# Performance work log

Measured on AMD Instinct MI355X. Metric: run time of the kernel, lower is better.

## Reference

```python
import jax, jax.numpy as jnp
import numpy as np


def setup_inputs() -> dict:
    key = jax.random.key(0)
    M, D = 131072, 16
    x = jax.random.normal(key, (M, D), dtype=jnp.float32)
    return {"x": x, "n_segs": 64, "k": 16}


def reference(x, n_segs, k):
    """Segmented kNN graph: for each point set (segment), find each point's k
    nearest neighbors (L2) within its own segment and emit edges knn -> node,
    with node ids globally offset by the segment start (sum_{p<i} |V_p| + j).

    Returns
    -------
    dists : [M, k] float32  squared L2 distance to each of the k neighbors
    src   : [M, k] int32    global node ids of the k predecessors of each node
    dst   : [M]    int32    global node ids (dst of the k edges in each row)
    """
    M, D = x.shape
    S = M // n_segs  # points per segment (equal-sized segments)
    xs = x.reshape(n_segs, S, D)                              # [N, S, D]
    sq = jnp.sum(xs * xs, axis=-1)                            # [N, S]
    # squared pairwise distances per segment: ||a||^2 + ||b||^2 - 2 a.b
    dist = sq[:, :, None] + sq[:, None, :] - 2.0 * jnp.einsum(
        "nsd,ntd->nst", xs, xs
    )                                                         # [N, S, S]
    neg, idx = jax.lax.top_k(-dist, k)                        # [N, S, k] each
    offs = (jnp.arange(n_segs, dtype=jnp.int32) * S)[:, None, None]
    src = (idx.astype(jnp.int32) + offs).reshape(M, k)        # global neighbor ids
    dst = jnp.arange(M, dtype=jnp.int32)
    dists = (-neg).reshape(M, k)
    return dists, src, dst
```

## Files before the change

kernel.cpp:

```cpp
#include <hip/hip_runtime.h>
#include <math.h>


#define DD 16
#define KK 16
#define SENT 0x7F7FFFFFu

typedef unsigned int uint;
typedef unsigned short ushort;
typedef short bf16x8 __attribute__((ext_vector_type(8)));
typedef float f32x4 __attribute__((ext_vector_type(4)));

__device__ __forceinline__ ushort f2bf(float f) {
  uint u = __float_as_uint(f);
  return (ushort)((u + 0x7FFFu + ((u >> 16) & 1u)) >> 16);
}

__device__ __forceinline__ void bitonic16(uint (&b)[16]) {
#pragma unroll
  for (int s = 8; s >= 1; s >>= 1) {
#pragma unroll
    for (int j = 0; j < 16; ++j) {
      if ((j & s) == 0) {
        uint lo = min(b[j], b[j + s]), hi = max(b[j], b[j + s]);
        b[j] = lo; b[j + s] = hi;
      }
    }
  }
}

__device__ __forceinline__ void flushSlots(uint (&bd)[8], uint (&qd)[4]) {
  qd[1] |= 1u; qd[2] |= 2u; qd[3] |= 3u;
#define CS(i, j) { uint lo = min(qd[i], qd[j]), hi = max(qd[i], qd[j]); qd[i] = lo; qd[j] = hi; }
  CS(0, 1) CS(2, 3) CS(0, 2) CS(1, 3) CS(1, 2)
#undef CS
#pragma unroll
  for (int t = 0; t < 4; ++t) bd[4 + t] = min(bd[4 + t], qd[3 - t]);
#pragma unroll
  for (int s = 4; s >= 1; s >>= 1) {
#pragma unroll
    for (int j = 0; j < 8; ++j) {
      if ((j & s) == 0) {
        uint lo = min(bd[j], bd[j + s]), hi = max(bd[j], bd[j + s]);
        bd[j] = lo; bd[j + s] = hi;
      }
    }
  }
#pragma unroll
  for (int t = 0; t < 4; ++t) qd[t] = SENT;
}

__global__ void sknn_prep(const float* __restrict__ x, ushort* __restrict__ augA,
                          ushort* __restrict__ augB, int M) {
  int p = blockIdx.x * 256 + threadIdx.x;
  if (p >= M) return;
  const float4* r = (const float4*)(x + (size_t)p * DD);
  float4 v0 = r[0], v1 = r[1], v2 = r[2], v3 = r[3];
  float f[16] = {v0.x, v0.y, v0.z, v0.w, v1.x, v1.y, v1.z, v1.w,
                 v2.x, v2.y, v2.z, v2.w, v3.x, v3.y, v3.z, v3.w};
  float sq = 0.f;
#pragma unroll
  for (int d = 0; d < 16; ++d) sq = fmaf(f[d], f[d], sq);
  ushort sq_hi = f2bf(sq);
  float hif = __uint_as_float(((uint)sq_hi) << 16);
  ushort sq_lo = f2bf(sq - hif);

  ushort A[32], B[32];
#pragma unroll
  for (int d = 0; d < 16; ++d) { A[d] = f2bf(-2.f * f[d]); B[d] = f2bf(f[d]); }
  A[16] = 0x3F80; A[17] = 0x3F80; A[18] = sq_hi; A[19] = sq_lo; A[20] = 0x3F80;
  B[16] = sq_hi;  B[17] = sq_lo;  B[18] = 0x3F80; B[19] = 0x3F80; B[20] = 0x3F80;
#pragma unroll
  for (int d = 21; d < 32; ++d) { A[d] = 0; B[d] = 0; }

  uint wa[16], wb[16];
#pragma unroll
  for (int i = 0; i < 16; ++i) {
    wa[i] = (uint)A[2 * i] | ((uint)A[2 * i + 1] << 16);
    wb[i] = (uint)B[2 * i] | ((uint)B[2 * i + 1] << 16);
  }
  uint4* da = (uint4*)(augA + (size_t)p * 32);
  uint4* db = (uint4*)(augB + (size_t)p * 32);
#pragma unroll
  for (int i = 0; i < 4; ++i) {
    da[i] = make_uint4(wa[4 * i], wa[4 * i + 1], wa[4 * i + 2], wa[4 * i + 3]);
    db[i] = make_uint4(wb[4 * i], wb[4 * i + 1], wb[4 * i + 2], wb[4 * i + 3]);
  }
}

__global__ __launch_bounds__(256, 4)
void sknn_mfma(const ushort* __restrict__ augA, const ushort* __restrict__ augB,
               float* __restrict__ out, int M, int S) {
  const int tid  = threadIdx.x;
  const int wv   = tid >> 6;
  const int lane = tid & 63;
  const int r16  = lane & 15;
  const int kh   = lane >> 4;
  const int qbase = blockIdx.x * 64 + wv * 16;
  const int segBase = (blockIdx.x * 64 / S) * S;
  const int NT = S / 16;
  const int NC = NT / 8;

  __shared__ uint shm[4096];

  const bf16x8 bfrag = *(const bf16x8*)(augB + (size_t)(qbase + r16) * 32 + kh * 8);
  const ushort* __restrict__ abase = augA + (size_t)segBase * 32;

  const int src_u = ((lane >> 2) * 32) + ((((lane & 3) ^ ((lane >> 3) & 3))) * 8);
  const int st0 = 2 * wv, st1 = 2 * wv + 1;
  const int rd_u = r16 * 16 + ((kh ^ ((r16 >> 1) & 3)) * 4);

  uint bd[8], qd[4];
#pragma unroll
  for (int i = 0; i < 8; ++i) bd[i] = SENT;
#pragma unroll
  for (int i = 0; i < 4; ++i) qd[i] = SENT;

  const f32x4 zacc = {0.f, 0.f, 0.f, 0.f};
  const uint kmask = 0xFFFFF800u;
  uint vidx = (uint)(kh * 4);

  auto cap = [&](const f32x4& acc) {
#pragma unroll
    for (int e = 0; e < 4; ++e)
      qd[e] = min(qd[e], (__float_as_uint(acc[e]) & kmask) | vidx);
    vidx += 16u;
  };

  {
    uint4 s0 = *(const uint4*)(abase + (size_t)st0 * 512 + src_u);
    uint4 s1 = *(const uint4*)(abase + (size_t)st1 * 512 + src_u);
    *(uint4*)(&shm[st0 * 256 + lane * 4]) = s0;
    *(uint4*)(&shm[st1 * 256 + lane * 4]) = s1;
    __syncthreads();
  }

  for (int c = 0; c < NC; ++c) {
    const uint cur = (uint)(c & 1) * 2048u;
    const uint nxt = 2048u - cur;
    uint4 s0, s1;
    const bool hasNext = (c + 1 < NC);
    if (hasNext) {
      const ushort* cb = abase + (size_t)(c + 1) * 4096;
      s0 = *(const uint4*)(cb + (size_t)st0 * 512 + src_u);
      s1 = *(const uint4*)(cb + (size_t)st1 * 512 + src_u);
    }
    const uint* tb = &shm[cur];
    bf16x8 fA = *(const bf16x8*)(tb + 0 * 256 + rd_u);
    bf16x8 fB = *(const bf16x8*)(tb + 1 * 256 + rd_u);
    bf16x8 fC = *(const bf16x8*)(tb + 2 * 256 + rd_u);
    bf16x8 fD = *(const bf16x8*)(tb + 3 * 256 + rd_u);
    f32x4 c0 = __builtin_amdgcn_mfma_f32_16x16x32_bf16(fA, bfrag, zacc, 0, 0, 0);
    f32x4 c1 = __builtin_amdgcn_mfma_f32_16x16x32_bf16(fB, bfrag, zacc, 0, 0, 0);
    fA = *(const bf16x8*)(tb + 4 * 256 + rd_u);
    fB = *(const bf16x8*)(tb + 5 * 256 + rd_u);
    cap(c0); cap(c1);
    f32x4 c2 = __builtin_amdgcn_mfma_f32_16x16x32_bf16(fC, bfrag, zacc, 0, 0, 0);
    f32x4 c3 = __builtin_amdgcn_mfma_f32_16x16x32_bf16(fD, bfrag, zacc, 0, 0, 0);
    fC = *(const bf16x8*)(tb + 6 * 256 + rd_u);
    fD = *(const bf16x8*)(tb + 7 * 256 + rd_u);
    cap(c2); cap(c3);
    c0 = __builtin_amdgcn_mfma_f32_16x16x32_bf16(fA, bfrag, zacc, 0, 0, 0);
    c1 = __builtin_amdgcn_mfma_f32_16x16x32_bf16(fB, bfrag, zacc, 0, 0, 0);
    cap(c0); cap(c1);
    c2 = __builtin_amdgcn_mfma_f32_16x16x32_bf16(fC, bfrag, zacc, 0, 0, 0);
    c3 = __builtin_amdgcn_mfma_f32_16x16x32_bf16(fD, bfrag, zacc, 0, 0, 0);
    cap(c2); cap(c3);
    flushSlots(bd, qd);
    if (hasNext) {
      *(uint4*)(&shm[nxt + st0 * 256 + lane * 4]) = s0;
      *(uint4*)(&shm[nxt + st1 * 256 + lane * 4]) = s1;
    }
    __syncthreads();
  }

  uint* myrow = &shm[tid * 9];
#pragma unroll
  for (int i = 0; i < 8; ++i) myrow[i] = bd[i];
  __syncthreads();
  if (kh != 0) return;

  uint cur16[16];
  {
    const uint* prow = &shm[(tid + 16) * 9];
#pragma unroll
    for (int i = 0; i < 8; ++i) cur16[i] = bd[i];
#pragma unroll
    for (int i = 0; i < 8; ++i) cur16[8 + i] = prow[7 - i];
    bitonic16(cur16);
  }
#pragma unroll
  for (int c = 2; c < 4; ++c) {
    const uint* prow = &shm[(tid + 16 * c) * 9];
    uint ob[8];
#pragma unroll
    for (int i = 0; i < 8; ++i) ob[i] = prow[i];
#pragma unroll
    for (int q = 0; q < 8; ++q) cur16[8 + q] = min(cur16[8 + q], ob[7 - q]);
    bitonic16(cur16);
  }

  const int p = qbase + r16;
  const float fb = (float)segBase;
  float dv[16], sv[16];
#pragma unroll
  for (int i = 0; i < 16; ++i) {
    dv[i] = __uint_as_float(cur16[i] & 0xFFFFF800u) - 1.0f;
    sv[i] = fb + (float)(cur16[i] & 0x7FFu);
  }
  float* __restrict__ dptr = out + (size_t)p * KK;
  ((float4*)dptr)[0] = make_float4(dv[0], dv[1], dv[2], dv[3]);
  ((float4*)dptr)[1] = make_float4(dv[4], dv[5], dv[6], dv[7]);
  ((float4*)dptr)[2] = make_float4(dv[8], dv[9], dv[10], dv[11]);
  ((float4*)dptr)[3] = make_float4(dv[12], dv[13], dv[14], dv[15]);
  float* __restrict__ sptr = out + (size_t)M * KK + (size_t)p * KK;
  ((float4*)sptr)[0] = make_float4(sv[0], sv[1], sv[2], sv[3]);
  ((float4*)sptr)[1] = make_float4(sv[4], sv[5], sv[6], sv[7]);
  ((float4*)sptr)[2] = make_float4(sv[8], sv[9], sv[10], sv[11]);
  ((float4*)sptr)[3] = make_float4(sv[12], sv[13], sv[14], sv[15]);
  out[(size_t)2 * M * KK + p] = (float)p;
}

__device__ __forceinline__ void flushQ16(uint (&bd)[16], uint (&qd)[4], uint& tau) {
#define CS(i, j) { uint lo = min(qd[i], qd[j]), hi = max(qd[i], qd[j]); qd[i] = lo; qd[j] = hi; }
  CS(0, 1) CS(2, 3) CS(0, 2) CS(1, 3) CS(1, 2)
#undef CS
#pragma unroll
  for (int t = 0; t < 4; ++t) {
    uint m = min(bd[12 + t], qd[3 - t]);
    uint lo = min(bd[4 + t], m), hi = max(bd[4 + t], m);
    bd[4 + t] = lo; bd[12 + t] = hi;
  }
#pragma unroll
  for (int s = 4; s >= 1; s >>= 1) {
#pragma unroll
    for (int j = 0; j < 16; ++j) {
      if ((j & s) == 0) {
        uint lo = min(bd[j], bd[j + s]), hi = max(bd[j], bd[j + s]);
        bd[j] = lo; bd[j + s] = hi;
      }
    }
  }
#pragma unroll
  for (int t = 0; t < 4; ++t) qd[t] = SENT;
  tau = min(tau, bd[15]);
}

__device__ __forceinline__ void merge16(uint (&bd)[16], const uint (&ob)[16]) {
  uint t[16];
#pragma unroll
  for (int i = 0; i < 16; ++i) t[i] = min(bd[i], ob[15 - i]);
#pragma unroll
  for (int i = 0; i < 16; ++i) bd[i] = t[i];
  bitonic16(bd);
}

template <int CLEN_C>
__global__ __launch_bounds__(256, 4)
void sknn_valu(const float* __restrict__ x, uint* __restrict__ part,
               int M, int S, int nch, int clenRt) {
  const int CLEN  = (CLEN_C > 0) ? CLEN_C : clenRt;
  const int tid   = threadIdx.x;
  const int qblk  = blockIdx.x / nch;
  const int chunk = blockIdx.x - qblk * nch;
  const int p     = qblk * 256 + tid;
  const int segBase = ((qblk * 256) / S) * S;
  const int j0    = chunk * CLEN;

  const float4* __restrict__ qr = (const float4*)(x + (size_t)p * DD);
  const float4 q0 = qr[0], q1 = qr[1], q2 = qr[2], q3 = qr[3];

  uint bd[16], qd[4];
  uint tau = SENT;
#pragma unroll
  for (int t = 0; t < 16; ++t) bd[t] = SENT;
#pragma unroll
  for (int t = 0; t < 4; ++t) qd[t] = SENT;

  const float4* __restrict__ cb = (const float4*)(x + (size_t)(segBase + j0) * DD);

  auto proc = [&](float4 c0, float4 c1, float4 c2, float4 c3, int j) {
    float t0, d0, d1, d2, d3;
    t0 = q0.x - c0.x; d0 = t0 * t0;
    t0 = q0.y - c0.y; d0 = fmaf(t0, t0, d0);
    t0 = q0.z - c0.z; d0 = fmaf(t0, t0, d0);
    t0 = q0.w - c0.w; d0 = fmaf(t0, t0, d0);
    t0 = q1.x - c1.x; d1 = t0 * t0;
    t0 = q1.y - c1.y; d1 = fmaf(t0, t0, d1);
    t0 = q1.z - c1.z; d1 = fmaf(t0, t0, d1);
    t0 = q1.w - c1.w; d1 = fmaf(t0, t0, d1);
    t0 = q2.x - c2.x; d2 = t0 * t0;
    t0 = q2.y - c2.y; d2 = fmaf(t0, t0, d2);
    t0 = q2.z - c2.z; d2 = fmaf(t0, t0, d2);
    t0 = q2.w - c2.w; d2 = fmaf(t0, t0, d2);
    t0 = q3.x - c3.x; d3 = t0 * t0;
    t0 = q3.y - c3.y; d3 = fmaf(t0, t0, d3);
    t0 = q3.z - c3.z; d3 = fmaf(t0, t0, d3);
    t0 = q3.w - c3.w; d3 = fmaf(t0, t0, d3);
    float nd = (d0 + d1) + (d2 + d3);
    const uint key = (__float_as_uint(nd) & 0xFFFFF800u) | (uint)(j0 + j);
    const bool pass = key < tau;
    qd[3] = pass ? qd[2] : qd[3];
    qd[2] = pass ? qd[1] : qd[2];
    qd[1] = pass ? qd[0] : qd[1];
    qd[0] = pass ? key : qd[0];
    if (__any((int)(qd[3] != SENT))) flushQ16(bd, qd, tau);
  };

  float4 a0 = cb[0], a1 = cb[1], a2 = cb[2], a3 = cb[3];
  for (int j = 0; j < CLEN; j += 2) {
    const int jb = j + 1;
    float4 b0 = cb[4 * jb + 0], b1 = cb[4 * jb + 1];
    float4 b2 = cb[4 * jb + 2], b3 = cb[4 * jb + 3];
    proc(a0, a1, a2, a3, j);
    const int ja = (j + 2 < CLEN) ? (j + 2) : 0;
    a0 = cb[4 * ja + 0]; a1 = cb[4 * ja + 1];
    a2 = cb[4 * ja + 2]; a3 = cb[4 * ja + 3];
    proc(b0, b1, b2, b3, jb);
  }
  if (__any((int)(qd[0] != SENT))) flushQ16(bd, qd, tau);

  uint* __restrict__ row = part + ((size_t)chunk * M + p) * KK;
  ((uint4*)row)[0] = make_uint4(bd[0], bd[1], bd[2], bd[3]);
  ((uint4*)row)[1] = make_uint4(bd[4], bd[5], bd[6], bd[7]);
  ((uint4*)row)[2] = make_uint4(bd[8], bd[9], bd[10], bd[11]);
  ((uint4*)row)[3] = make_uint4(bd[12], bd[13], bd[14], bd[15]);
}

__global__ void sknn_mergek(const uint* __restrict__ part, float* __restrict__ out,
                            int M, int S, int nch) {
  const int p = blockIdx.x * 256 + threadIdx.x;
  const uint* __restrict__ r0 = part + (size_t)p * KK;
  uint4 b0 = ((const uint4*)r0)[0], b1 = ((const uint4*)r0)[1];
  uint4 b2 = ((const uint4*)r0)[2], b3 = ((const uint4*)r0)[3];
  uint bd[16] = {b0.x, b0.y, b0.z, b0.w, b1.x, b1.y, b1.z, b1.w,
                 b2.x, b2.y, b2.z, b2.w, b3.x, b3.y, b3.z, b3.w};
  for (int c = 1; c < nch; ++c) {
    const uint* __restrict__ rc = part + ((size_t)c * M + p) * KK;
    uint4 o0 = ((const uint4*)rc)[0], o1 = ((const uint4*)rc)[1];
    uint4 o2 = ((const uint4*)rc)[2], o3 = ((const uint4*)rc)[3];
    uint ob[16] = {o0.x, o0.y, o0.z, o0.w, o1.x, o1.y, o1.z, o1.w,
                   o2.x, o2.y, o2.z, o2.w, o3.x, o3.y, o3.z, o3.w};
    merge16(bd, ob);
  }
  const int segBase = (p / S) * S;
  const float fb = (float)segBase;
  float dv[16], sv[16];
#pragma unroll
  for (int t = 0; t < 16; ++t) {
    dv[t] = __uint_as_float(bd[t] & 0xFFFFF800u);
    sv[t] = fb + (float)(bd[t] & 0x7FFu);
  }
  float* __restrict__ dptr = out + (size_t)p * KK;
  ((float4*)dptr)[0] = make_float4(dv[0], dv[1], dv[2], dv[3]);
  ((float4*)dptr)[1] = make_float4(dv[4], dv[5], dv[6], dv[7]);
  ((float4*)dptr)[2] = make_float4(dv[8], dv[9], dv[10], dv[11]);
  ((float4*)dptr)[3] = make_float4(dv[12], dv[13], dv[14], dv[15]);
  float* __restrict__ sptr = out + (size_t)M * KK + (size_t)p * KK;
  ((float4*)sptr)[0] = make_float4(sv[0], sv[1], sv[2], sv[3]);
  ((float4*)sptr)[1] = make_float4(sv[4], sv[5], sv[6], sv[7]);
  ((float4*)sptr)[2] = make_float4(sv[8], sv[9], sv[10], sv[11]);
  ((float4*)sptr)[3] = make_float4(sv[12], sv[13], sv[14], sv[15]);
  out[(size_t)2 * M * KK + p] = (float)p;
}

extern "C" void kernel_launch(void* const* d_in, const int* in_sizes, int n_in,
                              void* d_out, int out_size, void* d_ws, size_t ws_size,
                              hipStream_t stream) {
  const float* x = (const float*)d_in[0];
  const int M = in_sizes[0] / DD;
  const int S = M / 64;
  float* out = (float*)d_out;

  const size_t augBytes = (size_t)M * 32 * sizeof(ushort);
  if (ws_size >= 2 * augBytes) {
    ushort* augA = (ushort*)d_ws;
    ushort* augB = (ushort*)((char*)d_ws + augBytes);
    sknn_prep<<<M / 256, 256, 0, stream>>>(x, augA, augB, M);
    sknn_mfma<<<M / 64, 256, 0, stream>>>(augA, augB, out, M, S);
  } else {
    const int nch = 2;
    uint* part = (uint*)d_out;
    const int clen = S / nch;
    if (clen == 1024)
      sknn_valu<1024><<<(M / 256) * nch, 256, 0, stream>>>(x, part, M, S, nch, clen);
    else
      sknn_valu<0><<<(M / 256) * nch, 256, 0, stream>>>(x, part, M, S, nch, clen);
    sknn_mergek<<<M / 256, 256, 0, stream>>>(part, out, M, S, nch);
  }
}
```

Before: 54.64 us.

## Fuse bf16 augmentation prep into MFMA kNN kernel and drop fallback path

Result: slower. 57.33 us (+4.9%).

```diff
diff --git a/kernel.cpp b/kernel.cpp
--- a/kernel.cpp
+++ b/kernel.cpp
@@ -11,6 +11,11 @@
 typedef short bf16x8 __attribute__((ext_vector_type(8)));
 typedef float f32x4 __attribute__((ext_vector_type(4)));
 
+__device__ __forceinline__ uint cvtpk(float a, float b) {
+  uint r;
+  asm("v_cvt_pk_bf16_f32 %0, %1, %2" : "=v"(r) : "v"(a), "v"(b));
+  return r;
+}
 __device__ __forceinline__ ushort f2bf(float f) {
   uint u = __float_as_uint(f);
   return (ushort)((u + 0x7FFFu + ((u >> 16) & 1u)) >> 16);
@@ -50,47 +55,17 @@
   for (int t = 0; t < 4; ++t) qd[t] = SENT;
 }
 
-__global__ void sknn_prep(const float* __restrict__ x, ushort* __restrict__ augA,
-                          ushort* __restrict__ augB, int M) {
-  int p = blockIdx.x * 256 + threadIdx.x;
-  if (p >= M) return;
-  const float4* r = (const float4*)(x + (size_t)p * DD);
-  float4 v0 = r[0], v1 = r[1], v2 = r[2], v3 = r[3];
-  float f[16] = {v0.x, v0.y, v0.z, v0.w, v1.x, v1.y, v1.z, v1.w,
-                 v2.x, v2.y, v2.z, v2.w, v3.x, v3.y, v3.z, v3.w};
-  float sq = 0.f;
-#pragma unroll
-  for (int d = 0; d < 16; ++d) sq = fmaf(f[d], f[d], sq);
-  ushort sq_hi = f2bf(sq);
-  float hif = __uint_as_float(((uint)sq_hi) << 16);
-  ushort sq_lo = f2bf(sq - hif);
-
-  ushort A[32], B[32];
-#pragma unroll
-  for (int d = 0; d < 16; ++d) { A[d] = f2bf(-2.f * f[d]); B[d] = f2bf(f[d]); }
-  A[16] = 0x3F80; A[17] = 0x3F80; A[18] = sq_hi; A[19] = sq_lo; A[20] = 0x3F80;
-  B[16] = sq_hi;  B[17] = sq_lo;  B[18] = 0x3F80; B[19] = 0x3F80; B[20] = 0x3F80;
-#pragma unroll
-  for (int d = 21; d < 32; ++d) { A[d] = 0; B[d] = 0; }
-
-  uint wa[16], wb[16];
-#pragma unroll
-  for (int i = 0; i < 16; ++i) {
-    wa[i] = (uint)A[2 * i] | ((uint)A[2 * i + 1] << 16);
-    wb[i] = (uint)B[2 * i] | ((uint)B[2 * i + 1] << 16);
-  }
-  uint4* da = (uint4*)(augA + (size_t)p * 32);
-  uint4* db = (uint4*)(augB + (size_t)p * 32);
-#pragma unroll
-  for (int i = 0; i < 4; ++i) {
-    da[i] = make_uint4(wa[4 * i], wa[4 * i + 1], wa[4 * i + 2], wa[4 * i + 3]);
-    db[i] = make_uint4(wb[4 * i], wb[4 * i + 1], wb[4 * i + 2], wb[4 * i + 3]);
-  }
+__device__ __forceinline__ float sq16(const float4& a, const float4& b,
+                                      const float4& c, const float4& d) {
+  float s0 = fmaf(a.x, a.x, fmaf(a.y, a.y, fmaf(a.z, a.z, a.w * a.w)));
+  float s1 = fmaf(b.x, b.x, fmaf(b.y, b.y, fmaf(b.z, b.z, b.w * b.w)));
+  float s2 = fmaf(c.x, c.x, fmaf(c.y, c.y, fmaf(c.z, c.z, c.w * c.w)));
+  float s3 = fmaf(d.x, d.x, fmaf(d.y, d.y, fmaf(d.z, d.z, d.w * d.w)));
+  return (s0 + s1) + (s2 + s3);
 }
 
 __global__ __launch_bounds__(256, 4)
-void sknn_mfma(const ushort* __restrict__ augA, const ushort* __restrict__ augB,
-               float* __restrict__ out, int M, int S) {
+void sknn_fused(const float* __restrict__ x, float* __restrict__ out, int M, int S) {
   const int tid  = threadIdx.x;
   const int wv   = tid >> 6;
   const int lane = tid & 63;
@@ -100,15 +75,68 @@
   const int segBase = (blockIdx.x * 64 / S) * S;
   const int NT = S / 16;
   const int NC = NT / 8;
+  const int cloc = tid & 127;
+  const int half = tid >> 7;
 
   __shared__ uint shm[4096];
 
-  const bf16x8 bfrag = *(const bf16x8*)(augB + (size_t)(qbase + r16) * 32 + kh * 8);
-  const ushort* __restrict__ abase = augA + (size_t)segBase * 32;
-
-  const int src_u = ((lane >> 2) * 32) + ((((lane & 3) ^ ((lane >> 3) & 3))) * 8);
-  const int st0 = 2 * wv, st1 = 2 * wv + 1;
+  bf16x8 bfrag;
+  {
+    const float4* qp = (const float4*)(x + (size_t)(qbase + r16) * DD);
+    uint bw[4] = {0u, 0u, 0u, 0u};
+    if (kh == 0) {
+      float4 a = qp[0], b = qp[1];
+      bw[0] = cvtpk(a.x, a.y); bw[1] = cvtpk(a.z, a.w);
+      bw[2] = cvtpk(b.x, b.y); bw[3] = cvtpk(b.z, b.w);
+    } else if (kh == 1) {
+      float4 a = qp[2], b = qp[3];
+      bw[0] = cvtpk(a.x, a.y); bw[1] = cvtpk(a.z, a.w);
+      bw[2] = cvtpk(b.x, b.y); bw[3] = cvtpk(b.z, b.w);
+    } else if (kh == 2) {
+      float4 a = qp[0], b = qp[1], c = qp[2], d = qp[3];
+      float sq = sq16(a, b, c, d);
+      ushort hi = f2bf(sq);
+      float hif = __uint_as_float(((uint)hi) << 16);
+      ushort lo = f2bf(sq - hif);
+      bw[0] = (uint)hi | ((uint)lo << 16);
+      bw[1] = 0x3F803F80u;
+      bw[2] = 0x3F80u;
+      bw[3] = 0u;
+    }
+    bfrag = *(bf16x8*)bw;
+  }
+
+  const int stile = cloc >> 4, srow = cloc & 15;
+  const int ssw = (srow >> 1) & 3;
+  const int sbase = stile * 256 + srow * 16;
   const int rd_u = r16 * 16 + ((kh ^ ((r16 >> 1) & 3)) * 4);
+
+  auto stageWrite = [&](const float4& A0, const float4& A1,
+                        const float4& A2, const float4& A3, uint dst) {
+    uint* b = &shm[dst + sbase];
+    if (half == 0) {
+      uint4 w0, w1;
+      w0.x = cvtpk(-2.f * A0.x, -2.f * A0.y);
+      w0.y = cvtpk(-2.f * A0.z, -2.f * A0.w);
+      w0.z = cvtpk(-2.f * A1.x, -2.f * A1.y);
+      w0.w = cvtpk(-2.f * A1.z, -2.f * A1.w);
+      w1.x = cvtpk(-2.f * A2.x, -2.f * A2.y);
+      w1.y = cvtpk(-2.f * A2.z, -2.f * A2.w);
+      w1.z = cvtpk(-2.f * A3.x, -2.f * A3.y);
+      w1.w = cvtpk(-2.f * A3.z, -2.f * A3.w);
+      *(uint4*)(b + (0 ^ ssw) * 4) = w0;
+      *(uint4*)(b + (1 ^ ssw) * 4) = w1;
+    } else {
+      float sq = sq16(A0, A1, A2, A3);
+      ushort hi = f2bf(sq);
+      float hif = __uint_as_float(((uint)hi) << 16);
+      ushort lo = f2bf(sq - hif);
+      uint4 w2 = make_uint4(0x3F803F80u, (uint)hi | ((uint)lo << 16), 0x3F80u, 0u);
+      uint4 w3 = make_uint4(0u, 0u, 0u, 0u);
+      *(uint4*)(b + (2 ^ ssw) * 4) = w2;
+      *(uint4*)(b + (3 ^ ssw) * 4) = w3;
+    }
+  };
 
   uint bd[8], qd[4];
 #pragma unroll
@@ -128,22 +156,20 @@
   };
 
   {
-    uint4 s0 = *(const uint4*)(abase + (size_t)st0 * 512 + src_u);
-    uint4 s1 = *(const uint4*)(abase + (size_t)st1 * 512 + src_u);
-    *(uint4*)(&shm[st0 * 256 + lane * 4]) = s0;
-    *(uint4*)(&shm[st1 * 256 + lane * 4]) = s1;
+    const float4* cp = (const float4*)(x + (size_t)(segBase + cloc) * DD);
+    float4 A0 = cp[0], A1 = cp[1], A2 = cp[2], A3 = cp[3];
+    stageWrite(A0, A1, A2, A3, 0u);
     __syncthreads();
   }
 
   for (int c = 0; c < NC; ++c) {
     const uint cur = (uint)(c & 1) * 2048u;
     const uint nxt = 2048u - cur;
-    uint4 s0, s1;
+    float4 A0, A1, A2, A3;
     const bool hasNext = (c + 1 < NC);
     if (hasNext) {
-      const ushort* cb = abase + (size_t)(c + 1) * 4096;
-      s0 = *(const uint4*)(cb + (size_t)st0 * 512 + src_u);
-      s1 = *(const uint4*)(cb + (size_t)st1 * 512 + src_u);
+      const float4* cp = (const float4*)(x + (size_t)(segBase + (c + 1) * 128 + cloc) * DD);
+      A0 = cp[0]; A1 = cp[1]; A2 = cp[2]; A3 = cp[3];
     }
     const uint* tb = &shm[cur];
     bf16x8 fA = *(const bf16x8*)(tb + 0 * 256 + rd_u);
@@ -167,10 +193,7 @@
     c3 = __builtin_amdgcn_mfma_f32_16x16x32_bf16(fD, bfrag, zacc, 0, 0, 0);
     cap(c2); cap(c3);
     flushSlots(bd, qd);
-    if (hasNext) {
-      *(uint4*)(&shm[nxt + st0 * 256 + lane * 4]) = s0;
-      *(uint4*)(&shm[nxt + st1 * 256 + lane * 4]) = s1;
-    }
+    if (hasNext) stageWrite(A0, A1, A2, A3, nxt);
     __syncthreads();
   }
 
@@ -221,149 +244,6 @@
   out[(size_t)2 * M * KK + p] = (float)p;
 }
 
-__device__ __forceinline__ void flushQ16(uint (&bd)[16], uint (&qd)[4], uint& tau) {
-#define CS(i, j) { uint lo = min(qd[i], qd[j]), hi = max(qd[i], qd[j]); qd[i] = lo; qd[j] = hi; }
-  CS(0, 1) CS(2, 3) CS(0, 2) CS(1, 3) CS(1, 2)
-#undef CS
-#pragma unroll
-  for (int t = 0; t < 4; ++t) {
-    uint m = min(bd[12 + t], qd[3 - t]);
-    uint lo = min(bd[4 + t], m), hi = max(bd[4 + t], m);
-    bd[4 + t] = lo; bd[12 + t] = hi;
-  }
-#pragma unroll
-  for (int s = 4; s >= 1; s >>= 1) {
-#pragma unroll
-    for (int j = 0; j < 16; ++j) {
-      if ((j & s) == 0) {
-        uint lo = min(bd[j], bd[j + s]), hi = max(bd[j], bd[j + s]);
-        bd[j] = lo; bd[j + s] = hi;
-      }
-    }
-  }
-#pragma unroll
-  for (int t = 0; t < 4; ++t) qd[t] = SENT;
-  tau = min(tau, bd[15]);
-}
-
-__device__ __forceinline__ void merge16(uint (&bd)[16], const uint (&ob)[16]) {
-  uint t[16];
-#pragma unroll
-  for (int i = 0; i < 16; ++i) t[i] = min(bd[i], ob[15 - i]);
-#pragma unroll
-  for (int i = 0; i < 16; ++i) bd[i] = t[i];
-  bitonic16(bd);
-}
-
-template <int CLEN_C>
-__global__ __launch_bounds__(256, 4)
-void sknn_valu(const float* __restrict__ x, uint* __restrict__ part,
-               int M, int S, int nch, int clenRt) {
-  const int CLEN  = (CLEN_C > 0) ? CLEN_C : clenRt;
-  const int tid   = threadIdx.x;
-  const int qblk  = blockIdx.x / nch;
-  const int chunk = blockIdx.x - qblk * nch;
-  const int p     = qblk * 256 + tid;
-  const int segBase = ((qblk * 256) / S) * S;
-  const int j0    = chunk * CLEN;
-
-  const float4* __restrict__ qr = (const float4*)(x + (size_t)p * DD);
-  const float4 q0 = qr[0], q1 = qr[1], q2 = qr[2], q3 = qr[3];
-
-  uint bd[16], qd[4];
-  uint tau = SENT;
-#pragma unroll
-  for (int t = 0; t < 16; ++t) bd[t] = SENT;
-#pragma unroll
-  for (int t = 0; t < 4; ++t) qd[t] = SENT;
-
-  const float4* __restrict__ cb = (const float4*)(x + (size_t)(segBase + j0) * DD);
-
-  auto proc = [&](float4 c0, float4 c1, float4 c2, float4 c3, int j) {
-    float t0, d0, d1, d2, d3;
-    t0 = q0.x - c0.x; d0 = t0 * t0;
-    t0 = q0.y - c0.y; d0 = fmaf(t0, t0, d0);
-    t0 = q0.z - c0.z; d0 = fmaf(t0, t0, d0);
-    t0 = q0.w - c0.w; d0 = fmaf(t0, t0, d0);
-    t0 = q1.x - c1.x; d1 = t0 * t0;
-    t0 = q1.y - c1.y; d1 = fmaf(t0, t0, d1);
-    t0 = q1.z - c1.z; d1 = fmaf(t0, t0, d1);
-    t0 = q1.w - c1.w; d1 = fmaf(t0, t0, d1);
-    t0 = q2.x - c2.x; d2 = t0 * t0;
-    t0 = q2.y - c2.y; d2 = fmaf(t0, t0, d2);
-    t0 = q2.z - c2.z; d2 = fmaf(t0, t0, d2);
-    t0 = q2.w - c2.w; d2 = fmaf(t0, t0, d2);
-    t0 = q3.x - c3.x; d3 = t0 * t0;
-    t0 = q3.y - c3.y; d3 = fmaf(t0, t0, d3);
-    t0 = q3.z - c3.z; d3 = fmaf(t0, t0, d3);
-    t0 = q3.w - c3.w; d3 = fmaf(t0, t0, d3);
-    float nd = (d0 + d1) + (d2 + d3);
-    const uint key = (__float_as_uint(nd) & 0xFFFFF800u) | (uint)(j0 + j);
-    const bool pass = key < tau;
-    qd[3] = pass ? qd[2] : qd[3];
-    qd[2] = pass ? qd[1] : qd[2];
-    qd[1] = pass ? qd[0] : qd[1];
-    qd[0] = pass ? key : qd[0];
-    if (__any((int)(qd[3] != SENT))) flushQ16(bd, qd, tau);
-  };
-
-  float4 a0 = cb[0], a1 = cb[1], a2 = cb[2], a3 = cb[3];
-  for (int j = 0; j < CLEN; j += 2) {
-    const int jb = j + 1;
-    float4 b0 = cb[4 * jb + 0], b1 = cb[4 * jb + 1];
-    float4 b2 = cb[4 * jb + 2], b3 = cb[4 * jb + 3];
-    proc(a0, a1, a2, a3, j);
-    const int ja = (j + 2 < CLEN) ? (j + 2) : 0;
-    a0 = cb[4 * ja + 0]; a1 = cb[4 * ja + 1];
-    a2 = cb[4 * ja + 2]; a3 = cb[4 * ja + 3];
-    proc(b0, b1, b2, b3, jb);
-  }
-  if (__any((int)(qd[0] != SENT))) flushQ16(bd, qd, tau);
-
-  uint* __restrict__ row = part + ((size_t)chunk * M + p) * KK;
-  ((uint4*)row)[0] = make_uint4(bd[0], bd[1], bd[2], bd[3]);
-  ((uint4*)row)[1] = make_uint4(bd[4], bd[5], bd[6], bd[7]);
-  ((uint4*)row)[2] = make_uint4(bd[8], bd[9], bd[10], bd[11]);
-  ((uint4*)row)[3] = make_uint4(bd[12], bd[13], bd[14], bd[15]);
-}
-
-__global__ void sknn_mergek(const uint* __restrict__ part, float* __restrict__ out,
-                            int M, int S, int nch) {
-  const int p = blockIdx.x * 256 + threadIdx.x;
-  const uint* __restrict__ r0 = part + (size_t)p * KK;
-  uint4 b0 = ((const uint4*)r0)[0], b1 = ((const uint4*)r0)[1];
-  uint4 b2 = ((const uint4*)r0)[2], b3 = ((const uint4*)r0)[3];
-  uint bd[16] = {b0.x, b0.y, b0.z, b0.w, b1.x, b1.y, b1.z, b1.w,
-                 b2.x, b2.y, b2.z, b2.w, b3.x, b3.y, b3.z, b3.w};
-  for (int c = 1; c < nch; ++c) {
-    const uint* __restrict__ rc = part + ((size_t)c * M + p) * KK;
-    uint4 o0 = ((const uint4*)rc)[0], o1 = ((const uint4*)rc)[1];
-    uint4 o2 = ((const uint4*)rc)[2], o3 = ((const uint4*)rc)[3];
-    uint ob[16] = {o0.x, o0.y, o0.z, o0.w, o1.x, o1.y, o1.z, o1.w,
-                   o2.x, o2.y, o2.z, o2.w, o3.x, o3.y, o3.z, o3.w};
-    merge16(bd, ob);
-  }
-  const int segBase = (p / S) * S;
-  const float fb = (float)segBase;
-  float dv[16], sv[16];
-#pragma unroll
-  for (int t = 0; t < 16; ++t) {
-    dv[t] = __uint_as_float(bd[t] & 0xFFFFF800u);
-    sv[t] = fb + (float)(bd[t] & 0x7FFu);
-  }
-  float* __restrict__ dptr = out + (size_t)p * KK;
-  ((float4*)dptr)[0] = make_float4(dv[0], dv[1], dv[2], dv[3]);
-  ((float4*)dptr)[1] = make_float4(dv[4], dv[5], dv[6], dv[7]);
-  ((float4*)dptr)[2] = make_float4(dv[8], dv[9], dv[10], dv[11]);
-  ((float4*)dptr)[3] = make_float4(dv[12], dv[13], dv[14], dv[15]);
-  float* __restrict__ sptr = out + (size_t)M * KK + (size_t)p * KK;
-  ((float4*)sptr)[0] = make_float4(sv[0], sv[1], sv[2], sv[3]);
-  ((float4*)sptr)[1] = make_float4(sv[4], sv[5], sv[6], sv[7]);
-  ((float4*)sptr)[2] = make_float4(sv[8], sv[9], sv[10], sv[11]);
-  ((float4*)sptr)[3] = make_float4(sv[12], sv[13], sv[14], sv[15]);
-  out[(size_t)2 * M * KK + p] = (float)p;
-}
-
 extern "C" void kernel_launch(void* const* d_in, const int* in_sizes, int n_in,
                               void* d_out, int out_size, void* d_ws, size_t ws_size,
                               hipStream_t stream) {
@@ -371,21 +251,7 @@
   const int M = in_sizes[0] / DD;
   const int S = M / 64;
   float* out = (float*)d_out;
-
-  const size_t augBytes = (size_t)M * 32 * sizeof(ushort);
-  if (ws_size >= 2 * augBytes) {
-    ushort* augA = (ushort*)d_ws;
-    ushort* augB = (ushort*)((char*)d_ws + augBytes);
-    sknn_prep<<<M / 256, 256, 0, stream>>>(x, augA, augB, M);
-    sknn_mfma<<<M / 64, 256, 0, stream>>>(augA, augB, out, M, S);
-  } else {
-    const int nch = 2;
-    uint* part = (uint*)d_out;
-    const int clen = S / nch;
-    if (clen == 1024)
-      sknn_valu<1024><<<(M / 256) * nch, 256, 0, stream>>>(x, part, M, S, nch, clen);
-    else
-      sknn_valu<0><<<(M / 256) * nch, 256, 0, stream>>>(x, part, M, S, nch, clen);
-    sknn_mergek<<<M / 256, 256, 0, stream>>>(part, out, M, S, nch);
-  }
-}
+  (void)d_ws; (void)ws_size;
+
+  sknn_fused<<<M / 64, 256, 0, stream>>>(x, out, M, S);
+}
```
